# Performance work log

Measured on AMD Instinct MI355X. Metric: run time of the kernel, lower is better.

The kernel has to match this reference:

```python
import jax, jax.numpy as jnp
import numpy as np

ITER_ROUTING = 3
FINAL_LAMBDA = 0.01
EPS = 1e-9

N = 4
CHILD_SPACE = 12
KERNEL = 3
STRIDE = 1
CHILD_CAPS = 16
PARENT_CAPS = 32
POSE = 16


def _routing_map(child_space, k, s):
    # (child_space^2, parent_space^2) binary map: child c feeds parent p.
    parent_space = (child_space - k) // s + 1
    m = np.zeros((child_space * child_space, parent_space * parent_space), np.float32)
    for pr in range(parent_space):
        for pc in range(parent_space):
            p = pr * parent_space + pc
            for r in range(k):
                for c in range(k):
                    m[(pr * s + r) * child_space + (pc * s + c), p] = 1.0
    return m


def setup_inputs() -> dict:
    key = jax.random.key(0)
    k1, k2, k3, k4 = jax.random.split(key, 4)
    parent_space = (CHILD_SPACE - KERNEL) // STRIDE + 1
    kk = KERNEL * KERNEL
    votes = jax.random.normal(k1, (N * parent_space * parent_space, kk * CHILD_CAPS, PARENT_CAPS, POSE), jnp.float32)
    acts = jax.random.uniform(k2, (N * parent_space * parent_space, kk * CHILD_CAPS, 1), dtype=jnp.float32)
    beta_v = jax.random.normal(k3, (1, 1, 1, 1, PARENT_CAPS, 1), jnp.float32)
    beta_a = jax.random.normal(k4, (1, 1, 1, 1, PARENT_CAPS, 1), jnp.float32)
    srm = jnp.asarray(_routing_map(CHILD_SPACE, KERNEL, STRIDE))
    return {"votes_ij": votes, "activations_i": acts, "beta_v": beta_v, "beta_a": beta_a,
            "spatial_routing_matrix": srm, "batch_size": N, "kk": kk}


def _em_routing(votes_ij, activations_i, beta_v, beta_a, srm, batch_size, kk):
    Nb = batch_size
    C2, P2 = srm.shape  # child_space^2, parent_space^2
    P = int(round(P2 ** 0.5))
    K_total, O, ch = votes_ij.shape[1], votes_ij.shape[2], votes_ij.shape[3]
    child_caps = K_total // kk

    votes = votes_ij.reshape(Nb, P, P, K_total, O, ch)
    act_i = activations_i.reshape(Nb, P, P, K_total, 1, 1)

    # children per parent, ascending child index (stable argsort on -1/0 values)
    cidx = jnp.argsort(-srm, axis=0)[:kk].T           # (P2, kk)
    seg = cidx.reshape(-1)                            # (P2*kk,) child id per (parent, slot)
    ppc = jnp.sum(srm, axis=1)                        # parents-per-child, (C2,)
    # init_rr: 1 / (parents_per_child * parent_caps + 1e-9), gathered per parent slot
    rr0 = (1.0 / (ppc[cidx] * O + 1e-9)).reshape(1, P, P, kk, 1, 1)
    rr = jnp.broadcast_to(rr0, (1, P, P, kk, child_caps, O)).reshape(1, P, P, K_total, O, 1)

    layer_norm_factor = 100.0 / (float(K_total) / float(O))

    def m_step(rr, it):
        lam = FINAL_LAMBDA * (1.0 - 0.95 ** (it + 1))
        rr_prime = rr * act_i                                            # (N,P,P,K,O,1)
        rr_prime_sum = jnp.sum(rr_prime, axis=-3, keepdims=True)         # (N,P,P,1,O,1)
        mean_j = jnp.sum(rr_prime * votes, axis=-3, keepdims=True) / (rr_prime_sum + EPS)
        var_j = jnp.sum(rr_prime * jnp.square(votes - mean_j), axis=-3, keepdims=True) / (rr_prime_sum + EPS)
        cost_j_h = (beta_v + 0.5 * jnp.log(var_j + EPS)) * rr_prime_sum * layer_norm_factor
        cost_j = jnp.sum(cost_j_h, axis=-1, keepdims=True)               # (N,P,P,1,O,1)
        cost_mean = jnp.mean(cost_j, axis=-2, keepdims=True)
        cost_stdv = jnp.sqrt(jnp.sum(jnp.square(cost_j - cost_mean), axis=-2, keepdims=True) / O)
        act_j = jax.nn.sigmoid(lam * (beta_a + (cost_mean - cost_j) / (cost_stdv + EPS)))
        return act_j, mean_j, var_j

    def e_step(act_j, mean_j, var_j):
        # log N(vote; mean_j, var_j) per parent + log activation
        o_p0 = -jnp.sum(jnp.square(votes - mean_j) / (2.0 * var_j), axis=-1, keepdims=True)
        o_p2 = -0.5 * jnp.sum(jnp.log(2.0 * np.pi * var_j), axis=-1, keepdims=True)
        zz = jnp.log(act_j + EPS) + o_p0 + o_p2                          # (N,P,P,K,O,1)
        # softmax over ALL parents of each child (spatial kk slots x parent_caps),
        # done via segment reductions keyed by child id (== sparse/softmax/dense of original)
        z = jnp.moveaxis(zz.reshape(Nb, P2 * kk, child_caps, O), 1, 0)   # (P2*kk, N, cc, O)
        m = jax.ops.segment_max(jnp.max(z, axis=-1), seg, num_segments=C2)  # (C2, N, cc)
        m = jnp.where(jnp.isinf(m), 0.0, m)
        e = jnp.exp(z - m[seg][..., None])
        denom = jax.ops.segment_sum(jnp.sum(e, axis=-1), seg, num_segments=C2)
        rr_new = e / denom[seg][..., None]
        return jnp.moveaxis(rr_new, 0, 1).reshape(Nb, P, P, K_total, O, 1)

    for it in range(ITER_ROUTING):
        act_j, mean_j, var_j = m_step(rr, it)
        if it < ITER_ROUTING - 1:
            rr = e_step(act_j, mean_j, var_j)

    poses_j = mean_j[:, :, :, 0]        # (N,P,P,O,16)
    activations_j = act_j[:, :, :, 0]   # (N,P,P,O,1)
    return poses_j, activations_j


def reference(votes_ij, activations_i, beta_v, beta_a, spatial_routing_matrix, batch_size, kk):
    return _em_routing(votes_ij, activations_i, beta_v, beta_a, spatial_routing_matrix, batch_size, kk)
```

## Files before the change

### kernel.cpp

```cpp
#include <hip/hip_runtime.h>
#include <hip/hip_fp16.h>
#include <math.h>

#define NB     4
#define P      10
#define P2     100
#define CS     12
#define CCAPS  16
#define KTOT   144
#define O      32
#define POSE   16
#define VSZ    73728
#define EPSF   1e-9f
#define LNF    22.2222222222222222f
#define TWO_PI 6.28318530717958647f
#define NBP    400
#define EUNITS (NB*CS*CS*2)

#define LAM0 0.0005f
#define LAM1 0.000975f
#define LAM2 0.00142625f

__device__ float g_zz [NBP*KTOT*O];
__device__ float g_rrp[NBP*KTOT*O];

__device__ __forceinline__ int npar(int x) {
    int a = x + 1, b = CS - x;
    int m = a < 3 ? a : 3;
    return m < b ? m : b;
}

__global__ __launch_bounds__(1024, 8)
void v400_kernel(const float* __restrict__ votes, const float* __restrict__ acts,
                 __half* __restrict__ hv,
                 const float* __restrict__ beta_v, const float* __restrict__ beta_a,
                 float lam)
{
    __shared__ float  rr1[KTOT];
    __shared__ float4 lm1[1024];
    __shared__ float4 lm2[1024];
    __shared__ float  lss[1024];
    __shared__ float4 ml[128];
    __shared__ float4 il[128];
    __shared__ float  zl[O];
    __shared__ float  costl[O];
    __shared__ __align__(16) float zzl[KTOT*O];

    const int tid = threadIdx.x;
    const int bp  = blockIdx.x;
    const int p   = bp % P2;
    const int pr  = p / P, pc = p - pr * P;
    const int ks  = tid >> 7;
    const int q   = tid & 127;
    const int o   = q >> 2;
    const int c4  = q & 3;

    if (tid < KTOT) {
        int kslot = tid >> 4;
        int kr = kslot / 3, kc = kslot - kr * 3;
        float ppc = (float)(npar(pr + kr) * npar(pc + kc));
        rr1[tid] = acts[bp * KTOT + tid] / (ppc * 32.0f + EPSF);
    }
    __syncthreads();

    const float* vb = votes + (size_t)bp * VSZ + (size_t)(ks * 18) * 512 + q * 4;
    __half*      hb = hv    + (size_t)bp * VSZ + (size_t)(ks * 18) * 512 + q * 4;
    float  s  = 0.f;
    float4 m1 = make_float4(0.f, 0.f, 0.f, 0.f);
    float4 m2 = make_float4(0.f, 0.f, 0.f, 0.f);
    #pragma unroll 6
    for (int i = 0; i < 18; ++i) {
        float  rp = rr1[ks * 18 + i];
        float4 v  = *(const float4*)(vb + i * 512);
        s += rp;
        m1.x += rp * v.x;       m1.y += rp * v.y;
        m1.z += rp * v.z;       m1.w += rp * v.w;
        m2.x += rp * v.x * v.x; m2.y += rp * v.y * v.y;
        m2.z += rp * v.z * v.z; m2.w += rp * v.w * v.w;
        __half2 ha  = __floats2half2_rn(v.x, v.y);
        __half2 hbv = __floats2half2_rn(v.z, v.w);
        uint2 st;
        st.x = *(unsigned int*)&ha;
        st.y = *(unsigned int*)&hbv;
        *(uint2*)(hb + i * 512) = st;
    }
    lm1[tid] = m1; lm2[tid] = m2; lss[tid] = s;
    __syncthreads();

    float lv2 = 0.f, cost_o = 0.f;
    if (tid < 128) {
        m1 = lm1[tid]; m2 = lm2[tid]; s = lss[tid];
        #pragma unroll
        for (int w = 1; w < 8; ++w) {
            float4 a = lm1[w * 128 + tid];
            float4 b = lm2[w * 128 + tid];
            m1.x += a.x; m1.y += a.y; m1.z += a.z; m1.w += a.w;
            m2.x += b.x; m2.y += b.y; m2.z += b.z; m2.w += b.w;
            s += lss[w * 128 + tid];
        }

        float denom = s + EPSF;
        float4 mean = make_float4(m1.x/denom, m1.y/denom, m1.z/denom, m1.w/denom);
        float4 var;
        var.x = fmaxf(m2.x/denom - mean.x*mean.x, 1e-30f);
        var.y = fmaxf(m2.y/denom - mean.y*mean.y, 1e-30f);
        var.z = fmaxf(m2.z/denom - mean.z*mean.z, 1e-30f);
        var.w = fmaxf(m2.w/denom - mean.w*mean.w, 1e-30f);
        float4 i2 = make_float4(0.5f/var.x, 0.5f/var.y, 0.5f/var.z, 0.5f/var.w);
        ml[tid] = mean; il[tid] = i2;
        float lve = logf(var.x+EPSF)+logf(var.y+EPSF)+logf(var.z+EPSF)+logf(var.w+EPSF);
        float l2  = logf(TWO_PI*var.x)+logf(TWO_PI*var.y)+logf(TWO_PI*var.z)+logf(TWO_PI*var.w);
        lve += __shfl_xor(lve, 1); lve += __shfl_xor(lve, 2);
        l2  += __shfl_xor(l2, 1);  l2  += __shfl_xor(l2, 2);
        lv2 = l2;
        cost_o = (16.f * beta_v[o] + 0.5f * lve) * s * LNF;
        if (c4 == 0) costl[o] = cost_o;
    }
    __syncthreads();
    if (tid < 128) {
        float cm = 0.f;
        #pragma unroll
        for (int i = 0; i < O; ++i) cm += costl[i];
        cm *= (1.f / 32.f);
        float sq = 0.f;
        #pragma unroll
        for (int i = 0; i < O; ++i) { float d = costl[i] - cm; sq += d * d; }
        float cstd = sqrtf(sq * (1.f / 32.f));
        float aj = 1.f / (1.f + expf(-lam * (beta_a[o] + (cm - cost_o) / (cstd + EPSF))));
        if (c4 == 0) zl[o] = logf(aj + EPSF) - 0.5f * lv2;
    }
    __syncthreads();

    {
        float4 mean = ml[q];
        float4 iv   = il[q];
        float  zp   = zl[o];
        #pragma unroll 6
        for (int i = 0; i < 18; ++i) {
            float4 v = *(const float4*)(vb + i * 512);
            float dx = v.x - mean.x, dy = v.y - mean.y;
            float dz = v.z - mean.z, dw = v.w - mean.w;
            float t = dx*dx*iv.x + dy*dy*iv.y + dz*dz*iv.z + dw*dw*iv.w;
            t += __shfl_xor(t, 1); t += __shfl_xor(t, 2);
            if (c4 == 0) zzl[(ks * 18 + i) * O + o] = zp - t;
        }
    }
    __syncthreads();
    float4* dst = (float4*)(g_zz + (size_t)bp * (KTOT * O));
    for (int f = tid; f < KTOT * O / 4; f += 1024)
        dst[f] = ((float4*)zzl)[f];
}

template<bool LAST>
__global__ __launch_bounds__(1024, 8)
void m16_kernel(const __half* __restrict__ hv,
                const float* __restrict__ beta_v, const float* __restrict__ beta_a,
                float* __restrict__ out, float lam)
{
    __shared__ __align__(16) float rrp[KTOT*O];
    __shared__ float4 lm1[1024];
    __shared__ float4 lm2[1024];
    __shared__ float  lss[1024];
    __shared__ float4 ml[128];
    __shared__ float4 il[128];
    __shared__ float  zl[O];
    __shared__ float  costl[O];

    const int tid = threadIdx.x;
    const int bp  = blockIdx.x;
    const int ks  = tid >> 7;
    const int q   = tid & 127;
    const int o   = q >> 2;
    const int c4  = q & 3;

    for (int f = tid; f < KTOT * O / 4; f += 1024)
        ((float4*)rrp)[f] = ((const float4*)(g_rrp + (size_t)bp * (KTOT * O)))[f];
    __syncthreads();

    const __half* vb = hv + (size_t)bp * VSZ + (size_t)(ks * 18) * 512 + q * 4;
    float  s  = 0.f;
    float4 m1 = make_float4(0.f, 0.f, 0.f, 0.f);
    float4 m2 = make_float4(0.f, 0.f, 0.f, 0.f);
    #pragma unroll 6
    for (int i = 0; i < 18; ++i) {
        float rp = rrp[(ks * 18 + i) * O + o];
        uint2 u  = *(const uint2*)(vb + i * 512);
        float2 a = __half22float2(*(__half2*)&u.x);
        float2 b = __half22float2(*(__half2*)&u.y);
        s += rp;
        m1.x += rp * a.x;       m1.y += rp * a.y;
        m1.z += rp * b.x;       m1.w += rp * b.y;
        m2.x += rp * a.x * a.x; m2.y += rp * a.y * a.y;
        m2.z += rp * b.x * b.x; m2.w += rp * b.y * b.y;
    }
    lm1[tid] = m1; lm2[tid] = m2; lss[tid] = s;
    __syncthreads();

    float lv2 = 0.f, cost_o = 0.f;
    if (tid < 128) {
        m1 = lm1[tid]; m2 = lm2[tid]; s = lss[tid];
        #pragma unroll
        for (int w = 1; w < 8; ++w) {
            float4 a = lm1[w * 128 + tid];
            float4 b = lm2[w * 128 + tid];
            m1.x += a.x; m1.y += a.y; m1.z += a.z; m1.w += a.w;
            m2.x += b.x; m2.y += b.y; m2.z += b.z; m2.w += b.w;
            s += lss[w * 128 + tid];
        }

        float denom = s + EPSF;
        float4 mean = make_float4(m1.x/denom, m1.y/denom, m1.z/denom, m1.w/denom);
        float4 var;
        var.x = fmaxf(m2.x/denom - mean.x*mean.x, 1e-30f);
        var.y = fmaxf(m2.y/denom - mean.y*mean.y, 1e-30f);
        var.z = fmaxf(m2.z/denom - mean.z*mean.z, 1e-30f);
        var.w = fmaxf(m2.w/denom - mean.w*mean.w, 1e-30f);
        float4 i2 = make_float4(0.5f/var.x, 0.5f/var.y, 0.5f/var.z, 0.5f/var.w);
        ml[tid] = mean; il[tid] = i2;
        float lve = logf(var.x+EPSF)+logf(var.y+EPSF)+logf(var.z+EPSF)+logf(var.w+EPSF);
        float l2  = logf(TWO_PI*var.x)+logf(TWO_PI*var.y)+logf(TWO_PI*var.z)+logf(TWO_PI*var.w);
        lve += __shfl_xor(lve, 1); lve += __shfl_xor(lve, 2);
        l2  += __shfl_xor(l2, 1);  l2  += __shfl_xor(l2, 2);
        lv2 = l2;
        cost_o = (16.f * beta_v[o] + 0.5f * lve) * s * LNF;
        if (c4 == 0) costl[o] = cost_o;
    }
    __syncthreads();
    if (tid < 128) {
        float cm = 0.f;
        #pragma unroll
        for (int i = 0; i < O; ++i) cm += costl[i];
        cm *= (1.f / 32.f);
        float sq = 0.f;
        #pragma unroll
        for (int i = 0; i < O; ++i) { float d = costl[i] - cm; sq += d * d; }
        float cstd = sqrtf(sq * (1.f / 32.f));
        float aj = 1.f / (1.f + expf(-lam * (beta_a[o] + (cm - cost_o) / (cstd + EPSF))));
        if (LAST) {
            ((float4*)out)[bp * 128 + tid] = ml[tid];
            if (c4 == 0) out[(size_t)NBP * 512 + bp * O + o] = aj;
        } else {
            if (c4 == 0) zl[o] = logf(aj + EPSF) - 0.5f * lv2;
        }
    }
    if (LAST) return;
    __syncthreads();

    {
        float4 mean = ml[q];
        float4 iv   = il[q];
        float  zp   = zl[o];
        #pragma unroll 6
        for (int i = 0; i < 18; ++i) {
            uint2 u  = *(const uint2*)(vb + i * 512);
            float2 a = __half22float2(*(__half2*)&u.x);
            float2 b = __half22float2(*(__half2*)&u.y);
            float dx = a.x - mean.x, dy = a.y - mean.y;
            float dz = b.x - mean.z, dw = b.y - mean.w;
            float t = dx*dx*iv.x + dy*dy*iv.y + dz*dz*iv.z + dw*dw*iv.w;
            t += __shfl_xor(t, 1); t += __shfl_xor(t, 2);
            if (c4 == 0) rrp[(ks * 18 + i) * O + o] = zp - t;
        }
    }
    __syncthreads();
    float4* dst = (float4*)(g_zz + (size_t)bp * (KTOT * O));
    for (int f = tid; f < KTOT * O / 4; f += 1024)
        dst[f] = ((float4*)rrp)[f];
}

__global__ __launch_bounds__(256)
void e_kernel(const float* __restrict__ acts)
{
    const int tid = threadIdx.x;
    const int u   = blockIdx.x;
    const int b   = u / (CS * CS * 2);
    int r = u - b * (CS * CS * 2);
    const int child = r >> 1, half = r & 1;
    const int cr = child / CS, cl = child - cr * CS;
    const int cc = half * 8 + (tid >> 5), o = tid & 31;

    float zz[9];
    float vmax = -1e30f;
    #pragma unroll
    for (int kr = 0; kr < 3; ++kr) {
        int pr_ = cr - kr;
        #pragma unroll
        for (int kc = 0; kc < 3; ++kc) {
            int pc_ = cl - kc, si = kr * 3 + kc;
            float z = -1e30f;
            if (pr_ >= 0 && pr_ < P && pc_ >= 0 && pc_ < P) {
                int bpp = b * P2 + pr_ * P + pc_;
                z = g_zz[(size_t)bpp * (KTOT * O) + (si * CCAPS + cc) * O + o];
            }
            zz[si] = z;
            vmax = fmaxf(vmax, z);
        }
    }
    vmax = fmaxf(vmax, __shfl_xor(vmax, 1));
    vmax = fmaxf(vmax, __shfl_xor(vmax, 2));
    vmax = fmaxf(vmax, __shfl_xor(vmax, 4));
    vmax = fmaxf(vmax, __shfl_xor(vmax, 8));
    vmax = fmaxf(vmax, __shfl_xor(vmax, 16));

    float ps = 0.f;
    #pragma unroll
    for (int si = 0; si < 9; ++si) {
        float e = (zz[si] > -1e29f) ? expf(zz[si] - vmax) : 0.f;
        zz[si] = e;
        ps += e;
    }
    ps += __shfl_xor(ps, 1);
    ps += __shfl_xor(ps, 2);
    ps += __shfl_xor(ps, 4);
    ps += __shfl_xor(ps, 8);
    ps += __shfl_xor(ps, 16);
    float inv = 1.f / ps;

    #pragma unroll
    for (int kr = 0; kr < 3; ++kr) {
        int pr_ = cr - kr;
        #pragma unroll
        for (int kc = 0; kc < 3; ++kc) {
            int pc_ = cl - kc, si = kr * 3 + kc;
            if (pr_ >= 0 && pr_ < P && pc_ >= 0 && pc_ < P) {
                int bpp = b * P2 + pr_ * P + pc_;
                float av = acts[bpp * KTOT + si * CCAPS + cc];
                g_rrp[(size_t)bpp * (KTOT * O) + (si * CCAPS + cc) * O + o]
                    = zz[si] * inv * av;
            }
        }
    }
}

extern "C" void kernel_launch(void* const* d_in, const int* in_sizes, int n_in,
                              void* d_out, int out_size, void* d_ws, size_t ws_size,
                              hipStream_t stream)
{
    (void)in_sizes; (void)n_in; (void)out_size; (void)ws_size;

    const float* votes = (const float*)d_in[0];
    const float* acts  = (const float*)d_in[1];
    const float* bv    = (const float*)d_in[2];
    const float* ba    = (const float*)d_in[3];
    float* out = (float*)d_out;
    __half* hv = (__half*)d_ws;

    v400_kernel<<<dim3(NBP), dim3(1024), 0, stream>>>(votes, acts, hv, bv, ba, LAM0);
    e_kernel<<<dim3(EUNITS), dim3(256), 0, stream>>>(acts);
    m16_kernel<false><<<dim3(NBP), dim3(1024), 0, stream>>>(hv, bv, ba, out, LAM1);
    e_kernel<<<dim3(EUNITS), dim3(256), 0, stream>>>(acts);
    m16_kernel<true ><<<dim3(NBP), dim3(1024), 0, stream>>>(hv, bv, ba, out, LAM2);
}
```

Baseline: 251.4 us.

## Split each parent's M-step across two half-blocks and separate statistics from E-pass

```diff
diff --git a/kernel.cpp b/kernel.cpp
--- a/kernel.cpp
+++ b/kernel.cpp
@@ -15,14 +15,18 @@
 #define LNF    22.2222222222222222f
 #define TWO_PI 6.28318530717958647f
 #define NBP    400
+#define NBLK   800
 #define EUNITS (NB*CS*CS*2)
 
 #define LAM0 0.0005f
 #define LAM1 0.000975f
 #define LAM2 0.00142625f
 
-__device__ float g_zz [NBP*KTOT*O];
-__device__ float g_rrp[NBP*KTOT*O];
+__device__ float  g_zz [NBP*KTOT*O];
+__device__ float  g_rrp[NBP*KTOT*O];
+__device__ float4 g_pm1[NBLK*128];
+__device__ float4 g_pm2[NBLK*128];
+__device__ float  g_ps [NBLK*O];
 
 __device__ __forceinline__ int npar(int x) {
     int a = x + 1, b = CS - x;
@@ -30,41 +34,34 @@
     return m < b ? m : b;
 }
 
-__global__ __launch_bounds__(1024, 8)
-void v400_kernel(const float* __restrict__ votes, const float* __restrict__ acts,
-                 __half* __restrict__ hv,
-                 const float* __restrict__ beta_v, const float* __restrict__ beta_a,
-                 float lam)
-{
-    __shared__ float  rr1[KTOT];
-    __shared__ float4 lm1[1024];
-    __shared__ float4 lm2[1024];
-    __shared__ float  lss[1024];
-    __shared__ float4 ml[128];
-    __shared__ float4 il[128];
-    __shared__ float  zl[O];
-    __shared__ float  costl[O];
-    __shared__ __align__(16) float zzl[KTOT*O];
-
-    const int tid = threadIdx.x;
-    const int bp  = blockIdx.x;
+__global__ __launch_bounds__(512, 8)
+void a0_kernel(const float* __restrict__ votes, const float* __restrict__ acts,
+               __half* __restrict__ hv)
+{
+    __shared__ float  rr1[72];
+    __shared__ float4 lm1[512];
+    __shared__ float4 lm2[512];
+    __shared__ float  lss[512];
+
+    const int tid = threadIdx.x;
+    const int blk = blockIdx.x;
+    const int bp  = blk >> 1, h = blk & 1;
     const int p   = bp % P2;
     const int pr  = p / P, pc = p - pr * P;
     const int ks  = tid >> 7;
     const int q   = tid & 127;
-    const int o   = q >> 2;
-    const int c4  = q & 3;
-
-    if (tid < KTOT) {
-        int kslot = tid >> 4;
+
+    if (tid < 72) {
+        int row   = h * 72 + tid;
+        int kslot = row >> 4;
         int kr = kslot / 3, kc = kslot - kr * 3;
         float ppc = (float)(npar(pr + kr) * npar(pc + kc));
-        rr1[tid] = acts[bp * KTOT + tid] / (ppc * 32.0f + EPSF);
-    }
-    __syncthreads();
-
-    const float* vb = votes + (size_t)bp * VSZ + (size_t)(ks * 18) * 512 + q * 4;
-    __half*      hb = hv    + (size_t)bp * VSZ + (size_t)(ks * 18) * 512 + q * 4;
+        rr1[tid] = acts[bp * KTOT + row] / (ppc * 32.0f + EPSF);
+    }
+    __syncthreads();
+
+    const float* vb = votes + (size_t)bp * VSZ + (size_t)(h * 72 + ks * 18) * 512 + q * 4;
+    __half*      hb = hv    + (size_t)bp * VSZ + (size_t)(h * 72 + ks * 18) * 512 + q * 4;
     float  s  = 0.f;
     float4 m1 = make_float4(0.f, 0.f, 0.f, 0.f);
     float4 m2 = make_float4(0.f, 0.f, 0.f, 0.f);
@@ -87,17 +84,106 @@
     lm1[tid] = m1; lm2[tid] = m2; lss[tid] = s;
     __syncthreads();
 
+    if (tid < 128) {
+        float4 r1 = lm1[tid], r2 = lm2[tid];
+        float  sr = lss[tid];
+        #pragma unroll
+        for (int w = 1; w < 4; ++w) {
+            float4 a = lm1[w * 128 + tid];
+            float4 b = lm2[w * 128 + tid];
+            r1.x += a.x; r1.y += a.y; r1.z += a.z; r1.w += a.w;
+            r2.x += b.x; r2.y += b.y; r2.z += b.z; r2.w += b.w;
+            sr += lss[w * 128 + tid];
+        }
+        g_pm1[blk * 128 + tid] = r1;
+        g_pm2[blk * 128 + tid] = r2;
+        if ((tid & 3) == 0) g_ps[blk * O + (tid >> 2)] = sr;
+    }
+}
+
+__global__ __launch_bounds__(512, 8)
+void a16_kernel(const __half* __restrict__ hv)
+{
+    __shared__ float  rrp_s[72 * O];
+    __shared__ float4 lm1[512];
+    __shared__ float4 lm2[512];
+    __shared__ float  lss[512];
+
+    const int tid = threadIdx.x;
+    const int blk = blockIdx.x;
+    const int bp  = blk >> 1, h = blk & 1;
+    const int ks  = tid >> 7;
+    const int q   = tid & 127;
+    const int o   = q >> 2;
+
+    const float4* src = (const float4*)(g_rrp + (size_t)bp * (KTOT * O) + h * 72 * O);
+    for (int f = tid; f < 72 * O / 4; f += 512)
+        ((float4*)rrp_s)[f] = src[f];
+    __syncthreads();
+
+    const __half* vb = hv + (size_t)bp * VSZ + (size_t)(h * 72 + ks * 18) * 512 + q * 4;
+    float  s  = 0.f;
+    float4 m1 = make_float4(0.f, 0.f, 0.f, 0.f);
+    float4 m2 = make_float4(0.f, 0.f, 0.f, 0.f);
+    #pragma unroll 6
+    for (int i = 0; i < 18; ++i) {
+        float rp = rrp_s[(ks * 18 + i) * O + o];
+        uint2 u  = *(const uint2*)(vb + i * 512);
+        float2 a = __half22float2(*(__half2*)&u.x);
+        float2 b = __half22float2(*(__half2*)&u.y);
+        s += rp;
+        m1.x += rp * a.x;       m1.y += rp * a.y;
+        m1.z += rp * b.x;       m1.w += rp * b.y;
+        m2.x += rp * a.x * a.x; m2.y += rp * a.y * a.y;
+        m2.z += rp * b.x * b.x; m2.w += rp * b.y * b.y;
+    }
+    lm1[tid] = m1; lm2[tid] = m2; lss[tid] = s;
+    __syncthreads();
+
+    if (tid < 128) {
+        float4 r1 = lm1[tid], r2 = lm2[tid];
+        float  sr = lss[tid];
+        #pragma unroll
+        for (int w = 1; w < 4; ++w) {
+            float4 a = lm1[w * 128 + tid];
+            float4 b = lm2[w * 128 + tid];
+            r1.x += a.x; r1.y += a.y; r1.z += a.z; r1.w += a.w;
+            r2.x += b.x; r2.y += b.y; r2.z += b.z; r2.w += b.w;
+            sr += lss[w * 128 + tid];
+        }
+        g_pm1[blk * 128 + tid] = r1;
+        g_pm2[blk * 128 + tid] = r2;
+        if ((tid & 3) == 0) g_ps[blk * O + (tid >> 2)] = sr;
+    }
+}
+
+template<bool FPHALF>
+__global__ __launch_bounds__(512, 8)
+void b_kernel(const float* __restrict__ votes, const __half* __restrict__ hv,
+              const float* __restrict__ beta_v, const float* __restrict__ beta_a,
+              float lam)
+{
+    __shared__ float4 ml[128];
+    __shared__ float4 il[128];
+    __shared__ float  zl[O];
+    __shared__ float  costl[O];
+    __shared__ __align__(16) float zzl[72 * O];
+
+    const int tid = threadIdx.x;
+    const int blk = blockIdx.x;
+    const int bp  = blk >> 1, h = blk & 1;
+    const int ks  = tid >> 7;
+    const int q   = tid & 127;
+    const int o   = q >> 2;
+    const int c4  = q & 3;
+
     float lv2 = 0.f, cost_o = 0.f;
     if (tid < 128) {
-        m1 = lm1[tid]; m2 = lm2[tid]; s = lss[tid];
-        #pragma unroll
-        for (int w = 1; w < 8; ++w) {
-            float4 a = lm1[w * 128 + tid];
-            float4 b = lm2[w * 128 + tid];
-            m1.x += a.x; m1.y += a.y; m1.z += a.z; m1.w += a.w;
-            m2.x += b.x; m2.y += b.y; m2.z += b.z; m2.w += b.w;
-            s += lss[w * 128 + tid];
-        }
+        float4 a1 = g_pm1[(bp * 2) * 128 + tid], b1 = g_pm1[(bp * 2 + 1) * 128 + tid];
+        float4 a2 = g_pm2[(bp * 2) * 128 + tid], b2 = g_pm2[(bp * 2 + 1) * 128 + tid];
+        float4 m1 = make_float4(a1.x + b1.x, a1.y + b1.y, a1.z + b1.z, a1.w + b1.w);
+        float4 m2 = make_float4(a2.x + b2.x, a2.y + b2.y, a2.z + b2.z, a2.w + b2.w);
+        float  s  = g_ps[(bp * 2) * O + o] + g_ps[(bp * 2 + 1) * O + o];
 
         float denom = s + EPSF;
         float4 mean = make_float4(m1.x/denom, m1.y/denom, m1.z/denom, m1.w/denom);
@@ -135,137 +221,78 @@
         float4 mean = ml[q];
         float4 iv   = il[q];
         float  zp   = zl[o];
-        #pragma unroll 6
-        for (int i = 0; i < 18; ++i) {
-            float4 v = *(const float4*)(vb + i * 512);
-            float dx = v.x - mean.x, dy = v.y - mean.y;
-            float dz = v.z - mean.z, dw = v.w - mean.w;
-            float t = dx*dx*iv.x + dy*dy*iv.y + dz*dz*iv.z + dw*dw*iv.w;
-            t += __shfl_xor(t, 1); t += __shfl_xor(t, 2);
-            if (c4 == 0) zzl[(ks * 18 + i) * O + o] = zp - t;
-        }
-    }
-    __syncthreads();
-    float4* dst = (float4*)(g_zz + (size_t)bp * (KTOT * O));
-    for (int f = tid; f < KTOT * O / 4; f += 1024)
+        if (FPHALF) {
+            const __half* vb = hv + (size_t)bp * VSZ + (size_t)(h * 72 + ks * 18) * 512 + q * 4;
+            #pragma unroll 6
+            for (int i = 0; i < 18; ++i) {
+                uint2 u  = *(const uint2*)(vb + i * 512);
+                float2 a = __half22float2(*(__half2*)&u.x);
+                float2 b = __half22float2(*(__half2*)&u.y);
+                float dx = a.x - mean.x, dy = a.y - mean.y;
+                float dz = b.x - mean.z, dw = b.y - mean.w;
+                float t = dx*dx*iv.x + dy*dy*iv.y + dz*dz*iv.z + dw*dw*iv.w;
+                t += __shfl_xor(t, 1); t += __shfl_xor(t, 2);
+                if (c4 == 0) zzl[(ks * 18 + i) * O + o] = zp - t;
+            }
+        } else {
+            const float* vb = votes + (size_t)bp * VSZ + (size_t)(h * 72 + ks * 18) * 512 + q * 4;
+            #pragma unroll 6
+            for (int i = 0; i < 18; ++i) {
+                float4 v = *(const float4*)(vb + i * 512);
+                float dx = v.x - mean.x, dy = v.y - mean.y;
+                float dz = v.z - mean.z, dw = v.w - mean.w;
+                float t = dx*dx*iv.x + dy*dy*iv.y + dz*dz*iv.z + dw*dw*iv.w;
+                t += __shfl_xor(t, 1); t += __shfl_xor(t, 2);
+                if (c4 == 0) zzl[(ks * 18 + i) * O + o] = zp - t;
+            }
+        }
+    }
+    __syncthreads();
+    float4* dst = (float4*)(g_zz + (size_t)bp * (KTOT * O) + h * 72 * O);
+    for (int f = tid; f < 72 * O / 4; f += 512)
         dst[f] = ((float4*)zzl)[f];
 }
 
-template<bool LAST>
-__global__ __launch_bounds__(1024, 8)
-void m16_kernel(const __half* __restrict__ hv,
-                const float* __restrict__ beta_v, const float* __restrict__ beta_a,
-                float* __restrict__ out, float lam)
-{
-    __shared__ __align__(16) float rrp[KTOT*O];
-    __shared__ float4 lm1[1024];
-    __shared__ float4 lm2[1024];
-    __shared__ float  lss[1024];
-    __shared__ float4 ml[128];
-    __shared__ float4 il[128];
-    __shared__ float  zl[O];
-    __shared__ float  costl[O];
-
+__global__ __launch_bounds__(128)
+void bfin_kernel(const float* __restrict__ beta_v, const float* __restrict__ beta_a,
+                 float* __restrict__ out, float lam)
+{
+    __shared__ float costl[O];
     const int tid = threadIdx.x;
     const int bp  = blockIdx.x;
-    const int ks  = tid >> 7;
-    const int q   = tid & 127;
-    const int o   = q >> 2;
-    const int c4  = q & 3;
-
-    for (int f = tid; f < KTOT * O / 4; f += 1024)
-        ((float4*)rrp)[f] = ((const float4*)(g_rrp + (size_t)bp * (KTOT * O)))[f];
-    __syncthreads();
-
-    const __half* vb = hv + (size_t)bp * VSZ + (size_t)(ks * 18) * 512 + q * 4;
-    float  s  = 0.f;
-    float4 m1 = make_float4(0.f, 0.f, 0.f, 0.f);
-    float4 m2 = make_float4(0.f, 0.f, 0.f, 0.f);
-    #pragma unroll 6
-    for (int i = 0; i < 18; ++i) {
-        float rp = rrp[(ks * 18 + i) * O + o];
-        uint2 u  = *(const uint2*)(vb + i * 512);
-        float2 a = __half22float2(*(__half2*)&u.x);
-        float2 b = __half22float2(*(__half2*)&u.y);
-        s += rp;
-        m1.x += rp * a.x;       m1.y += rp * a.y;
-        m1.z += rp * b.x;       m1.w += rp * b.y;
-        m2.x += rp * a.x * a.x; m2.y += rp * a.y * a.y;
-        m2.z += rp * b.x * b.x; m2.w += rp * b.y * b.y;
-    }
-    lm1[tid] = m1; lm2[tid] = m2; lss[tid] = s;
-    __syncthreads();
-
-    float lv2 = 0.f, cost_o = 0.f;
-    if (tid < 128) {
-        m1 = lm1[tid]; m2 = lm2[tid]; s = lss[tid];
-        #pragma unroll
-        for (int w = 1; w < 8; ++w) {
-            float4 a = lm1[w * 128 + tid];
-            float4 b = lm2[w * 128 + tid];
-            m1.x += a.x; m1.y += a.y; m1.z += a.z; m1.w += a.w;
-            m2.x += b.x; m2.y += b.y; m2.z += b.z; m2.w += b.w;
-            s += lss[w * 128 + tid];
-        }
-
-        float denom = s + EPSF;
-        float4 mean = make_float4(m1.x/denom, m1.y/denom, m1.z/denom, m1.w/denom);
-        float4 var;
-        var.x = fmaxf(m2.x/denom - mean.x*mean.x, 1e-30f);
-        var.y = fmaxf(m2.y/denom - mean.y*mean.y, 1e-30f);
-        var.z = fmaxf(m2.z/denom - mean.z*mean.z, 1e-30f);
-        var.w = fmaxf(m2.w/denom - mean.w*mean.w, 1e-30f);
-        float4 i2 = make_float4(0.5f/var.x, 0.5f/var.y, 0.5f/var.z, 0.5f/var.w);
-        ml[tid] = mean; il[tid] = i2;
-        float lve = logf(var.x+EPSF)+logf(var.y+EPSF)+logf(var.z+EPSF)+logf(var.w+EPSF);
-        float l2  = logf(TWO_PI*var.x)+logf(TWO_PI*var.y)+logf(TWO_PI*var.z)+logf(TWO_PI*var.w);
-        lve += __shfl_xor(lve, 1); lve += __shfl_xor(lve, 2);
-        l2  += __shfl_xor(l2, 1);  l2  += __shfl_xor(l2, 2);
-        lv2 = l2;
-        cost_o = (16.f * beta_v[o] + 0.5f * lve) * s * LNF;
-        if (c4 == 0) costl[o] = cost_o;
-    }
-    __syncthreads();
-    if (tid < 128) {
-        float cm = 0.f;
-        #pragma unroll
-        for (int i = 0; i < O; ++i) cm += costl[i];
-        cm *= (1.f / 32.f);
-        float sq = 0.f;
-        #pragma unroll
-        for (int i = 0; i < O; ++i) { float d = costl[i] - cm; sq += d * d; }
-        float cstd = sqrtf(sq * (1.f / 32.f));
-        float aj = 1.f / (1.f + expf(-lam * (beta_a[o] + (cm - cost_o) / (cstd + EPSF))));
-        if (LAST) {
-            ((float4*)out)[bp * 128 + tid] = ml[tid];
-            if (c4 == 0) out[(size_t)NBP * 512 + bp * O + o] = aj;
-        } else {
-            if (c4 == 0) zl[o] = logf(aj + EPSF) - 0.5f * lv2;
-        }
-    }
-    if (LAST) return;
-    __syncthreads();
-
-    {
-        float4 mean = ml[q];
-        float4 iv   = il[q];
-        float  zp   = zl[o];
-        #pragma unroll 6
-        for (int i = 0; i < 18; ++i) {
-            uint2 u  = *(const uint2*)(vb + i * 512);
-            float2 a = __half22float2(*(__half2*)&u.x);
-            float2 b = __half22float2(*(__half2*)&u.y);
-            float dx = a.x - mean.x, dy = a.y - mean.y;
-            float dz = b.x - mean.z, dw = b.y - mean.w;
-            float t = dx*dx*iv.x + dy*dy*iv.y + dz*dz*iv.z + dw*dw*iv.w;
-            t += __shfl_xor(t, 1); t += __shfl_xor(t, 2);
-            if (c4 == 0) rrp[(ks * 18 + i) * O + o] = zp - t;
-        }
-    }
-    __syncthreads();
-    float4* dst = (float4*)(g_zz + (size_t)bp * (KTOT * O));
-    for (int f = tid; f < KTOT * O / 4; f += 1024)
-        dst[f] = ((float4*)rrp)[f];
+    const int o   = tid >> 2, c4 = tid & 3;
+
+    float4 a1 = g_pm1[(bp * 2) * 128 + tid], b1 = g_pm1[(bp * 2 + 1) * 128 + tid];
+    float4 a2 = g_pm2[(bp * 2) * 128 + tid], b2 = g_pm2[(bp * 2 + 1) * 128 + tid];
+    float4 m1 = make_float4(a1.x + b1.x, a1.y + b1.y, a1.z + b1.z, a1.w + b1.w);
+    float4 m2 = make_float4(a2.x + b2.x, a2.y + b2.y, a2.z + b2.z, a2.w + b2.w);
+    float  s  = g_ps[(bp * 2) * O + o] + g_ps[(bp * 2 + 1) * O + o];
+
+    float denom = s + EPSF;
+    float4 mean = make_float4(m1.x/denom, m1.y/denom, m1.z/denom, m1.w/denom);
+    float4 var;
+    var.x = fmaxf(m2.x/denom - mean.x*mean.x, 1e-30f);
+    var.y = fmaxf(m2.y/denom - mean.y*mean.y, 1e-30f);
+    var.z = fmaxf(m2.z/denom - mean.z*mean.z, 1e-30f);
+    var.w = fmaxf(m2.w/denom - mean.w*mean.w, 1e-30f);
+    float lve = logf(var.x+EPSF)+logf(var.y+EPSF)+logf(var.z+EPSF)+logf(var.w+EPSF);
+    lve += __shfl_xor(lve, 1); lve += __shfl_xor(lve, 2);
+    float cost_o = (16.f * beta_v[o] + 0.5f * lve) * s * LNF;
+    if (c4 == 0) costl[o] = cost_o;
+    __syncthreads();
+
+    float cm = 0.f;
+    #pragma unroll
+    for (int i = 0; i < O; ++i) cm += costl[i];
+    cm *= (1.f / 32.f);
+    float sq = 0.f;
+    #pragma unroll
+    for (int i = 0; i < O; ++i) { float d = costl[i] - cm; sq += d * d; }
+    float cstd = sqrtf(sq * (1.f / 32.f));
+    float aj = 1.f / (1.f + expf(-lam * (beta_a[o] + (cm - cost_o) / (cstd + EPSF))));
+
+    ((float4*)out)[bp * 128 + tid] = mean;
+    if (c4 == 0) out[(size_t)NBP * 512 + bp * O + o] = aj;
 }
 
 __global__ __launch_bounds__(256)
@@ -345,9 +372,12 @@
     float* out = (float*)d_out;
     __half* hv = (__half*)d_ws;
 
-    v400_kernel<<<dim3(NBP), dim3(1024), 0, stream>>>(votes, acts, hv, bv, ba, LAM0);
-    e_kernel<<<dim3(EUNITS), dim3(256), 0, stream>>>(acts);
-    m16_kernel<false><<<dim3(NBP), dim3(1024), 0, stream>>>(hv, bv, ba, out, LAM1);
-    e_kernel<<<dim3(EUNITS), dim3(256), 0, stream>>>(acts);
-    m16_kernel<true ><<<dim3(NBP), dim3(1024), 0, stream>>>(hv, bv, ba, out, LAM2);
-}
+    a0_kernel        <<<dim3(NBLK),   dim3(512), 0, stream>>>(votes, acts, hv);
+    b_kernel<false>  <<<dim3(NBLK),   dim3(512), 0, stream>>>(votes, hv, bv, ba, LAM0);
+    e_kernel         <<<dim3(EUNITS), dim3(256), 0, stream>>>(acts);
+    a16_kernel       <<<dim3(NBLK),   dim3(512), 0, stream>>>(hv);
+    b_kernel<true>   <<<dim3(NBLK),   dim3(512), 0, stream>>>(votes, hv, bv, ba, LAM1);
+    e_kernel         <<<dim3(EUNITS), dim3(256), 0, stream>>>(acts);
+    a16_kernel       <<<dim3(NBLK),   dim3(512), 0, stream>>>(hv);
+    bfin_kernel      <<<dim3(NBP),    dim3(128), 0, stream>>>(bv, ba, out, LAM2);
+}
```

New measurement: 268.6 us. 6.9% more time.

## Halve block size, alias shared buffers, and reread fp16 votes in first pass

Applied to the files above, without the earlier changes.

```diff
diff --git a/kernel.cpp b/kernel.cpp
--- a/kernel.cpp
+++ b/kernel.cpp
@@ -30,21 +30,22 @@
     return m < b ? m : b;
 }
 
-__global__ __launch_bounds__(1024, 8)
+__global__ __launch_bounds__(512)
 void v400_kernel(const float* __restrict__ votes, const float* __restrict__ acts,
                  __half* __restrict__ hv,
                  const float* __restrict__ beta_v, const float* __restrict__ beta_a,
                  float lam)
 {
+    __shared__ __align__(16) unsigned char smem[18432];
+    float4* lm1 = (float4*)smem;
+    float4* lm2 = (float4*)(smem + 8192);
+    float*  lss = (float*) (smem + 16384);
+    float*  zzl = (float*) smem;
     __shared__ float  rr1[KTOT];
-    __shared__ float4 lm1[1024];
-    __shared__ float4 lm2[1024];
-    __shared__ float  lss[1024];
     __shared__ float4 ml[128];
     __shared__ float4 il[128];
     __shared__ float  zl[O];
     __shared__ float  costl[O];
-    __shared__ __align__(16) float zzl[KTOT*O];
 
     const int tid = threadIdx.x;
     const int bp  = blockIdx.x;
@@ -63,14 +64,14 @@
     }
     __syncthreads();
 
-    const float* vb = votes + (size_t)bp * VSZ + (size_t)(ks * 18) * 512 + q * 4;
-    __half*      hb = hv    + (size_t)bp * VSZ + (size_t)(ks * 18) * 512 + q * 4;
+    const float* vb = votes + (size_t)bp * VSZ + (size_t)(ks * 36) * 512 + q * 4;
+    __half*      hb = hv    + (size_t)bp * VSZ + (size_t)(ks * 36) * 512 + q * 4;
     float  s  = 0.f;
     float4 m1 = make_float4(0.f, 0.f, 0.f, 0.f);
     float4 m2 = make_float4(0.f, 0.f, 0.f, 0.f);
     #pragma unroll 6
-    for (int i = 0; i < 18; ++i) {
-        float  rp = rr1[ks * 18 + i];
+    for (int i = 0; i < 36; ++i) {
+        float  rp = rr1[ks * 36 + i];
         float4 v  = *(const float4*)(vb + i * 512);
         s += rp;
         m1.x += rp * v.x;       m1.y += rp * v.y;
@@ -91,7 +92,7 @@
     if (tid < 128) {
         m1 = lm1[tid]; m2 = lm2[tid]; s = lss[tid];
         #pragma unroll
-        for (int w = 1; w < 8; ++w) {
+        for (int w = 1; w < 4; ++w) {
             float4 a = lm1[w * 128 + tid];
             float4 b = lm2[w * 128 + tid];
             m1.x += a.x; m1.y += a.y; m1.z += a.z; m1.w += a.w;
@@ -136,31 +137,35 @@
         float4 iv   = il[q];
         float  zp   = zl[o];
         #pragma unroll 6
-        for (int i = 0; i < 18; ++i) {
-            float4 v = *(const float4*)(vb + i * 512);
-            float dx = v.x - mean.x, dy = v.y - mean.y;
-            float dz = v.z - mean.z, dw = v.w - mean.w;
+        for (int i = 0; i < 36; ++i) {
+            uint2 u  = *(const uint2*)(hb + i * 512);
+            float2 a = __half22float2(*(__half2*)&u.x);
+            float2 b = __half22float2(*(__half2*)&u.y);
+            float dx = a.x - mean.x, dy = a.y - mean.y;
+            float dz = b.x - mean.z, dw = b.y - mean.w;
             float t = dx*dx*iv.x + dy*dy*iv.y + dz*dz*iv.z + dw*dw*iv.w;
             t += __shfl_xor(t, 1); t += __shfl_xor(t, 2);
-            if (c4 == 0) zzl[(ks * 18 + i) * O + o] = zp - t;
+            if (c4 == 0) zzl[(ks * 36 + i) * O + o] = zp - t;
         }
     }
     __syncthreads();
     float4* dst = (float4*)(g_zz + (size_t)bp * (KTOT * O));
-    for (int f = tid; f < KTOT * O / 4; f += 1024)
+    for (int f = tid; f < KTOT * O / 4; f += 512)
         dst[f] = ((float4*)zzl)[f];
 }
 
 template<bool LAST>
-__global__ __launch_bounds__(1024, 8)
+__global__ __launch_bounds__(512)
 void m16_kernel(const __half* __restrict__ hv,
                 const float* __restrict__ beta_v, const float* __restrict__ beta_a,
                 float* __restrict__ out, float lam)
 {
-    __shared__ __align__(16) float rrp[KTOT*O];
-    __shared__ float4 lm1[1024];
-    __shared__ float4 lm2[1024];
-    __shared__ float  lss[1024];
+    __shared__ __align__(16) unsigned char smem[18432];
+    float*  rrp = (float*) smem;
+    float4* lm1 = (float4*)smem;
+    float4* lm2 = (float4*)(smem + 8192);
+    float*  lss = (float*) (smem + 16384);
+    float*  zzl = (float*) smem;
     __shared__ float4 ml[128];
     __shared__ float4 il[128];
     __shared__ float  zl[O];
@@ -173,17 +178,17 @@
     const int o   = q >> 2;
     const int c4  = q & 3;
 
-    for (int f = tid; f < KTOT * O / 4; f += 1024)
+    for (int f = tid; f < KTOT * O / 4; f += 512)
         ((float4*)rrp)[f] = ((const float4*)(g_rrp + (size_t)bp * (KTOT * O)))[f];
     __syncthreads();
 
-    const __half* vb = hv + (size_t)bp * VSZ + (size_t)(ks * 18) * 512 + q * 4;
+    const __half* vb = hv + (size_t)bp * VSZ + (size_t)(ks * 36) * 512 + q * 4;
     float  s  = 0.f;
     float4 m1 = make_float4(0.f, 0.f, 0.f, 0.f);
     float4 m2 = make_float4(0.f, 0.f, 0.f, 0.f);
     #pragma unroll 6
-    for (int i = 0; i < 18; ++i) {
-        float rp = rrp[(ks * 18 + i) * O + o];
+    for (int i = 0; i < 36; ++i) {
+        float rp = rrp[(ks * 36 + i) * O + o];
         uint2 u  = *(const uint2*)(vb + i * 512);
         float2 a = __half22float2(*(__half2*)&u.x);
         float2 b = __half22float2(*(__half2*)&u.y);
@@ -193,6 +198,7 @@
         m2.x += rp * a.x * a.x; m2.y += rp * a.y * a.y;
         m2.z += rp * b.x * b.x; m2.w += rp * b.y * b.y;
     }
+    __syncthreads();
     lm1[tid] = m1; lm2[tid] = m2; lss[tid] = s;
     __syncthreads();
 
@@ -200,7 +206,7 @@
     if (tid < 128) {
         m1 = lm1[tid]; m2 = lm2[tid]; s = lss[tid];
         #pragma unroll
-        for (int w = 1; w < 8; ++w) {
+        for (int w = 1; w < 4; ++w) {
             float4 a = lm1[w * 128 + tid];
             float4 b = lm2[w * 128 + tid];
             m1.x += a.x; m1.y += a.y; m1.z += a.z; m1.w += a.w;
@@ -251,7 +257,7 @@
         float4 iv   = il[q];
         float  zp   = zl[o];
         #pragma unroll 6
-        for (int i = 0; i < 18; ++i) {
+        for (int i = 0; i < 36; ++i) {
             uint2 u  = *(const uint2*)(vb + i * 512);
             float2 a = __half22float2(*(__half2*)&u.x);
             float2 b = __half22float2(*(__half2*)&u.y);
@@ -259,13 +265,13 @@
             float dz = b.x - mean.z, dw = b.y - mean.w;
             float t = dx*dx*iv.x + dy*dy*iv.y + dz*dz*iv.z + dw*dw*iv.w;
             t += __shfl_xor(t, 1); t += __shfl_xor(t, 2);
-            if (c4 == 0) rrp[(ks * 18 + i) * O + o] = zp - t;
+            if (c4 == 0) zzl[(ks * 36 + i) * O + o] = zp - t;
         }
     }
     __syncthreads();
     float4* dst = (float4*)(g_zz + (size_t)bp * (KTOT * O));
-    for (int f = tid; f < KTOT * O / 4; f += 1024)
-        dst[f] = ((float4*)rrp)[f];
+    for (int f = tid; f < KTOT * O / 4; f += 512)
+        dst[f] = ((float4*)zzl)[f];
 }
 
 __global__ __launch_bounds__(256)
@@ -345,9 +351,9 @@
     float* out = (float*)d_out;
     __half* hv = (__half*)d_ws;
 
-    v400_kernel<<<dim3(NBP), dim3(1024), 0, stream>>>(votes, acts, hv, bv, ba, LAM0);
+    v400_kernel<<<dim3(NBP), dim3(512), 0, stream>>>(votes, acts, hv, bv, ba, LAM0);
     e_kernel<<<dim3(EUNITS), dim3(256), 0, stream>>>(acts);
-    m16_kernel<false><<<dim3(NBP), dim3(1024), 0, stream>>>(hv, bv, ba, out, LAM1);
+    m16_kernel<false><<<dim3(NBP), dim3(512), 0, stream>>>(hv, bv, ba, out, LAM1);
     e_kernel<<<dim3(EUNITS), dim3(256), 0, stream>>>(acts);
-    m16_kernel<true ><<<dim3(NBP), dim3(1024), 0, stream>>>(hv, bv, ba, out, LAM2);
-}
+    m16_kernel<true ><<<dim3(NBP), dim3(512), 0, stream>>>(hv, bv, ba, out, LAM2);
+}
```

Result: slower. 264.1 us (+5.1%).
